# Performance work log

Measured on AMD Instinct MI355X. Metric: run time of the kernel, lower is better.

Reference implementation:

```python
import jax, jax.numpy as jnp
import numpy as np

N, IN, OUT, T = 65536, 256, 256, 8


def setup_inputs() -> dict:
    key = jax.random.key(0)
    k1, k2, k3, k4 = jax.random.split(key, 4)
    x = jax.random.normal(k1, (N, IN), dtype=jnp.float32)
    types = jax.random.randint(k2, (N,), 0, T, dtype=jnp.int32)
    # xavier_uniform for W: limit = sqrt(6 / (fan_in + fan_out)) with fan computed
    # on the last two dims (out_size, in_size)
    limit = float(np.sqrt(6.0 / (IN + OUT)))
    W = jax.random.uniform(k3, (T, OUT, IN), dtype=jnp.float32, minval=-limit, maxval=limit)
    # original inits b to zeros; use small random values so the bias path is exercised
    b = 0.01 * jax.random.normal(k4, (T, OUT), dtype=jnp.float32)
    return {"x": x, "types": types, "W": W, "b": b}


def reference(x, types, W, b):
    # out[i] = W[types[i]] @ x[i] + b[types[i]]
    # Grouped-GEMM expressed as a loop over the small fixed set of types,
    # avoiding the huge [N, OUT, IN] gather of W[types].
    num_types = W.shape[0]
    out = b[types]  # [N, OUT]
    for t in range(num_types):
        mask = (types == t)[:, None]  # [N, 1]
        out = out + jnp.where(mask, x @ W[t].T, jnp.float32(0.0))
    return out
```

## Files before the change

### kernel.cpp

```cpp
#include <hip/hip_runtime.h>
#include <stdint.h>


#define NROWS 65536
#define NTYPES 8
#define KDIM 256
#define ODIM 256
#define BM 32
#define MAX_TILES (NROWS / BM + NTYPES)

typedef __attribute__((ext_vector_type(8))) short short8;
typedef __attribute__((ext_vector_type(4))) float f32x4;

__device__ __forceinline__ unsigned short f2bf(float f) {
    unsigned int u = __float_as_uint(f);
    u += 0x7fffu + ((u >> 16) & 1u);
    return (unsigned short)(u >> 16);
}

__global__ void prep_bucket_kernel(const float* __restrict__ W,
                                   unsigned short* __restrict__ Wp,
                                   const int* __restrict__ types,
                                   int* __restrict__ cnt,
                                   int* __restrict__ idx) {
    const int b = blockIdx.x;
    if (b < 256) {
        const int gid = b * 256 + threadIdx.x;
        const int R   = gid >> 5;
        const int c32 = gid & 31;
        const int t  = R >> 8;
        const int r  = R & 255;
        const int f  = r >> 4;
        const int rr = r & 15;
        const int q  = c32 >> 2;
        const int l  = (c32 & 3) * 16 + rr;
        const float* src = W + (size_t)R * KDIM + c32 * 8;
        const float4 v0 = *(const float4*)src;
        const float4 v1 = *(const float4*)(src + 4);
        ushort4 p0, p1;
        p0.x = f2bf(v0.x); p0.y = f2bf(v0.y); p0.z = f2bf(v0.z); p0.w = f2bf(v0.w);
        p1.x = f2bf(v1.x); p1.y = f2bf(v1.y); p1.z = f2bf(v1.z); p1.w = f2bf(v1.w);
        ushort4* dst = (ushort4*)(Wp + (size_t)(((t * 16 + f) * 8 + q) * 512 + l * 8));
        dst[0] = p0; dst[1] = p1;
    } else {
        __shared__ int h[NTYPES];
        __shared__ int base[NTYPES];
        int i = (b - 256) * 256 + threadIdx.x;
        if (threadIdx.x < NTYPES) h[threadIdx.x] = 0;
        __syncthreads();
        int t = types[i];
        int r = atomicAdd(&h[t], 1);
        __syncthreads();
        if (threadIdx.x < NTYPES)
            base[threadIdx.x] = atomicAdd(&cnt[threadIdx.x], h[threadIdx.x]);
        __syncthreads();
        idx[t * NROWS + base[t] + r] = i;
    }
}

__global__ __launch_bounds__(256, 5)
void gemm_kernel(const float* __restrict__ x,
                 const float* __restrict__ bias,
                 const unsigned short* __restrict__ Wp,
                 const int* __restrict__ cnt,
                 const int* __restrict__ idx,
                 float* __restrict__ out) {
    const int bid = blockIdx.x;
    int t = -1, m0 = 0, count = 0, accum = 0;
    #pragma unroll
    for (int i = 0; i < NTYPES; ++i) {
        int c = cnt[i];
        int ntile = (c + BM - 1) / BM;
        if (t < 0 && bid < accum + ntile) { t = i; m0 = (bid - accum) * BM; count = c; }
        accum += ntile;
    }
    if (t < 0) return;

    __shared__ unsigned short As[BM * KDIM];
    __shared__ int idx_s[BM];
    char* AsB = (char*)As;

    const int tid = threadIdx.x;
    const int srow = tid >> 3;
    const int sc   = tid & 7;

    {
        const int gr = m0 + srow;
        const int xr = idx[t * NROWS + (gr < count ? gr : count - 1)];
        if (sc == 0) idx_s[srow] = xr;
        const float* xs = x + (size_t)xr * KDIM;
        float4 av[8];
        #pragma unroll
        for (int s = 0; s < 8; ++s)
            av[s] = *(const float4*)(xs + (s * 8 + sc) * 4);
        #pragma unroll
        for (int s = 0; s < 8; ++s) {
            const int slot = s * 8 + sc;
            ushort4 pk;
            pk.x = f2bf(av[s].x); pk.y = f2bf(av[s].y);
            pk.z = f2bf(av[s].z); pk.w = f2bf(av[s].w);
            const int c = slot >> 1;
            *(ushort4*)(AsB + srow * 512 + ((c ^ (srow & 7)) * 16) + (slot & 1) * 8) = pk;
        }
    }
    __syncthreads();

    const int wave = tid >> 6;
    const int lane = tid & 63;
    const int lr = lane & 15;
    const int lq = lane >> 4;

    const unsigned short* Wpt = Wp + (size_t)t * 16 * 8 * 512;

    f32x4 acc[2][4] = {};

    #pragma unroll
    for (int q = 0; q < 8; ++q) {
        short8 bf[4], af[2];
        #pragma unroll
        for (int j = 0; j < 4; ++j)
            bf[j] = *(const short8*)(Wpt + ((size_t)((wave * 4 + j) * 8 + q)) * 512
                                         + lane * 8);
        #pragma unroll
        for (int i = 0; i < 2; ++i) {
            const int row = i * 16 + lr;
            af[i] = *(const short8*)(AsB + row * 512
                                         + (((q << 2) + lq) ^ (row & 7)) * 16);
        }
        #pragma unroll
        for (int i = 0; i < 2; ++i)
            #pragma unroll
            for (int j = 0; j < 4; ++j)
                acc[i][j] = __builtin_amdgcn_mfma_f32_16x16x32_bf16(
                    af[i], bf[j], acc[i][j], 0, 0, 0);
    }

    float bv[4];
    #pragma unroll
    for (int j = 0; j < 4; ++j)
        bv[j] = bias[t * ODIM + wave * 64 + j * 16 + lr];

    #pragma unroll
    for (int i = 0; i < 2; ++i) {
        #pragma unroll
        for (int r = 0; r < 4; ++r) {
            const int lm = i * 16 + lq * 4 + r;
            const int gr = m0 + lm;
            if (gr < count) {
                const size_t orow = (size_t)idx_s[lm] * ODIM;
                #pragma unroll
                for (int j = 0; j < 4; ++j)
                    __builtin_nontemporal_store(
                        acc[i][j][r] + bv[j],
                        &out[orow + wave * 64 + j * 16 + lr]);
            }
        }
    }
}

extern "C" void kernel_launch(void* const* d_in, const int* in_sizes, int n_in,
                              void* d_out, int out_size, void* d_ws, size_t ws_size,
                              hipStream_t stream) {
    const float* x     = (const float*)d_in[0];
    const int*   types = (const int*)d_in[1];
    const float* W     = (const float*)d_in[2];
    const float* b     = (const float*)d_in[3];
    float* out = (float*)d_out;

    char* ws = (char*)d_ws;
    int* cnt = (int*)ws;
    int* idx = (int*)(ws + 1024);
    unsigned short* Wp = (unsigned short*)(ws + 1024 + (size_t)NTYPES * NROWS * sizeof(int));

    hipMemsetAsync(cnt, 0, NTYPES * sizeof(int), stream);
    prep_bucket_kernel<<<512, 256, 0, stream>>>(W, Wp, types, cnt, idx);
    gemm_kernel<<<MAX_TILES, 256, 0, stream>>>(x, b, Wp, cnt, idx, out);
}
```

Before: 135.3 us.

## Replace global type bucketing with per-block local sort over contiguous row tiles

New measurement: 143.3 us. 5.9% more time.

```diff
diff --git a/kernel.cpp b/kernel.cpp
--- a/kernel.cpp
+++ b/kernel.cpp
@@ -6,8 +6,9 @@
 #define NTYPES 8
 #define KDIM 256
 #define ODIM 256
-#define BM 32
-#define MAX_TILES (NROWS / BM + NTYPES)
+#define RPB 128
+#define NBLK (NROWS / RPB)
+#define MAXFRAG 16
 
 typedef __attribute__((ext_vector_type(8))) short short8;
 typedef __attribute__((ext_vector_type(4))) float f32x4;
@@ -18,141 +19,147 @@
     return (unsigned short)(u >> 16);
 }
 
-__global__ void prep_bucket_kernel(const float* __restrict__ W,
-                                   unsigned short* __restrict__ Wp,
-                                   const int* __restrict__ types,
-                                   int* __restrict__ cnt,
-                                   int* __restrict__ idx) {
-    const int b = blockIdx.x;
-    if (b < 256) {
-        const int gid = b * 256 + threadIdx.x;
-        const int R   = gid >> 5;
-        const int c32 = gid & 31;
-        const int t  = R >> 8;
-        const int r  = R & 255;
-        const int f  = r >> 4;
-        const int rr = r & 15;
-        const int q  = c32 >> 2;
-        const int l  = (c32 & 3) * 16 + rr;
-        const float* src = W + (size_t)R * KDIM + c32 * 8;
-        const float4 v0 = *(const float4*)src;
-        const float4 v1 = *(const float4*)(src + 4);
-        ushort4 p0, p1;
-        p0.x = f2bf(v0.x); p0.y = f2bf(v0.y); p0.z = f2bf(v0.z); p0.w = f2bf(v0.w);
-        p1.x = f2bf(v1.x); p1.y = f2bf(v1.y); p1.z = f2bf(v1.z); p1.w = f2bf(v1.w);
-        ushort4* dst = (ushort4*)(Wp + (size_t)(((t * 16 + f) * 8 + q) * 512 + l * 8));
-        dst[0] = p0; dst[1] = p1;
-    } else {
-        __shared__ int h[NTYPES];
-        __shared__ int base[NTYPES];
-        int i = (b - 256) * 256 + threadIdx.x;
-        if (threadIdx.x < NTYPES) h[threadIdx.x] = 0;
-        __syncthreads();
-        int t = types[i];
-        int r = atomicAdd(&h[t], 1);
-        __syncthreads();
-        if (threadIdx.x < NTYPES)
-            base[threadIdx.x] = atomicAdd(&cnt[threadIdx.x], h[threadIdx.x]);
-        __syncthreads();
-        idx[t * NROWS + base[t] + r] = i;
-    }
+__global__ void prep_pack_kernel(const float* __restrict__ W,
+                                 unsigned short* __restrict__ Wp) {
+    const int gid = blockIdx.x * 256 + threadIdx.x;
+    const int R   = gid >> 5;
+    const int c32 = gid & 31;
+    const int t  = R >> 8;
+    const int r  = R & 255;
+    const int f  = r >> 4;
+    const int rr = r & 15;
+    const int q  = c32 >> 2;
+    const int l  = (c32 & 3) * 16 + rr;
+    const float* src = W + (size_t)R * KDIM + c32 * 8;
+    const float4 v0 = *(const float4*)src;
+    const float4 v1 = *(const float4*)(src + 4);
+    ushort4 p0, p1;
+    p0.x = f2bf(v0.x); p0.y = f2bf(v0.y); p0.z = f2bf(v0.z); p0.w = f2bf(v0.w);
+    p1.x = f2bf(v1.x); p1.y = f2bf(v1.y); p1.z = f2bf(v1.z); p1.w = f2bf(v1.w);
+    ushort4* dst = (ushort4*)(Wp + (size_t)(((t * 16 + f) * 8 + q) * 512 + l * 8));
+    dst[0] = p0; dst[1] = p1;
 }
 
-__global__ __launch_bounds__(256, 5)
+__global__ __launch_bounds__(256, 2)
 void gemm_kernel(const float* __restrict__ x,
                  const float* __restrict__ bias,
                  const unsigned short* __restrict__ Wp,
-                 const int* __restrict__ cnt,
-                 const int* __restrict__ idx,
+                 const int* __restrict__ types,
                  float* __restrict__ out) {
-    const int bid = blockIdx.x;
-    int t = -1, m0 = 0, count = 0, accum = 0;
-    #pragma unroll
-    for (int i = 0; i < NTYPES; ++i) {
-        int c = cnt[i];
-        int ntile = (c + BM - 1) / BM;
-        if (t < 0 && bid < accum + ntile) { t = i; m0 = (bid - accum) * BM; count = c; }
-        accum += ntile;
-    }
-    if (t < 0) return;
+    const int w0 = blockIdx.x * RPB;
 
-    __shared__ unsigned short As[BM * KDIM];
-    __shared__ int idx_s[BM];
+    __shared__ unsigned short As[RPB * KDIM];
+    __shared__ int perm[RPB];
+    __shared__ int hist[NTYPES];
+    __shared__ int base_[NTYPES];
+    __shared__ int ftype[MAXFRAG];
+    __shared__ int fbase[MAXFRAG];
+    __shared__ int fcnt_[MAXFRAG];
+    __shared__ int nfrag_s;
     char* AsB = (char*)As;
 
     const int tid = threadIdx.x;
-    const int srow = tid >> 3;
-    const int sc   = tid & 7;
+
+    if (tid < NTYPES) hist[tid] = 0;
+    __syncthreads();
+
+    int myt = 0, myrank = 0;
+    if (tid < RPB) {
+        myt = types[w0 + tid];
+        myrank = atomicAdd(&hist[myt], 1);
+    }
 
     {
-        const int gr = m0 + srow;
-        const int xr = idx[t * NROWS + (gr < count ? gr : count - 1)];
-        if (sc == 0) idx_s[srow] = xr;
-        const float* xs = x + (size_t)xr * KDIM;
-        float4 av[8];
+        const int srow = tid >> 1;
+        const int sh   = tid & 1;
+        const float* xs = x + (size_t)(w0 + srow) * KDIM + sh * 128;
         #pragma unroll
-        for (int s = 0; s < 8; ++s)
-            av[s] = *(const float4*)(xs + (s * 8 + sc) * 4);
-        #pragma unroll
-        for (int s = 0; s < 8; ++s) {
-            const int slot = s * 8 + sc;
-            ushort4 pk;
-            pk.x = f2bf(av[s].x); pk.y = f2bf(av[s].y);
-            pk.z = f2bf(av[s].z); pk.w = f2bf(av[s].w);
-            const int c = slot >> 1;
-            *(ushort4*)(AsB + srow * 512 + ((c ^ (srow & 7)) * 16) + (slot & 1) * 8) = pk;
+        for (int rnd = 0; rnd < 4; ++rnd) {
+            float4 av[8];
+            #pragma unroll
+            for (int s = 0; s < 8; ++s)
+                av[s] = *(const float4*)(xs + (rnd * 8 + s) * 4);
+            #pragma unroll
+            for (int s = 0; s < 8; ++s) {
+                const int slot = sh * 32 + rnd * 8 + s;
+                ushort4 pk;
+                pk.x = f2bf(av[s].x); pk.y = f2bf(av[s].y);
+                pk.z = f2bf(av[s].z); pk.w = f2bf(av[s].w);
+                const int c = slot >> 1;
+                *(ushort4*)(AsB + srow * 512 + ((c ^ (srow & 7)) * 16)
+                            + (slot & 1) * 8) = pk;
+            }
         }
     }
+    __syncthreads();
+
+    if (tid == 0) {
+        int acc = 0, nf = 0;
+        #pragma unroll
+        for (int t2 = 0; t2 < NTYPES; ++t2) {
+            base_[t2] = acc;
+            const int c = hist[t2];
+            for (int f = 0; f < c; f += 16) {
+                ftype[nf] = t2;
+                fbase[nf] = acc + f;
+                fcnt_[nf] = (c - f < 16) ? (c - f) : 16;
+                ++nf;
+            }
+            acc += c;
+        }
+        nfrag_s = nf;
+    }
+    __syncthreads();
+    if (tid < RPB) perm[base_[myt] + myrank] = tid;
     __syncthreads();
 
     const int wave = tid >> 6;
     const int lane = tid & 63;
     const int lr = lane & 15;
     const int lq = lane >> 4;
+    const int nfrag = nfrag_s;
 
-    const unsigned short* Wpt = Wp + (size_t)t * 16 * 8 * 512;
+    short8 bf[8][4];
+    float bv[4];
+    int cur_t = -1;
 
-    f32x4 acc[2][4] = {};
-
-    #pragma unroll
-    for (int q = 0; q < 8; ++q) {
-        short8 bf[4], af[2];
-        #pragma unroll
-        for (int j = 0; j < 4; ++j)
-            bf[j] = *(const short8*)(Wpt + ((size_t)((wave * 4 + j) * 8 + q)) * 512
-                                         + lane * 8);
-        #pragma unroll
-        for (int i = 0; i < 2; ++i) {
-            const int row = i * 16 + lr;
-            af[i] = *(const short8*)(AsB + row * 512
-                                         + (((q << 2) + lq) ^ (row & 7)) * 16);
-        }
-        #pragma unroll
-        for (int i = 0; i < 2; ++i)
+    for (int fi = 0; fi < nfrag; ++fi) {
+        const int t = ftype[fi];
+        if (t != cur_t) {
+            const unsigned short* wbase = Wp + (size_t)t * (16 * 8 * 512)
+                                             + (size_t)(wave * 4) * 8 * 512 + lane * 8;
+            #pragma unroll
+            for (int q = 0; q < 8; ++q)
+                #pragma unroll
+                for (int j = 0; j < 4; ++j)
+                    bf[q][j] = *(const short8*)(wbase + j * 4096 + q * 512);
             #pragma unroll
             for (int j = 0; j < 4; ++j)
-                acc[i][j] = __builtin_amdgcn_mfma_f32_16x16x32_bf16(
-                    af[i], bf[j], acc[i][j], 0, 0, 0);
-    }
+                bv[j] = bias[t * ODIM + wave * 64 + j * 16 + lr];
+            cur_t = t;
+        }
+        const int fb = fbase[fi], fc = fcnt_[fi];
+        const int arow = perm[fb + (lr < fc ? lr : 0)];
 
-    float bv[4];
-    #pragma unroll
-    for (int j = 0; j < 4; ++j)
-        bv[j] = bias[t * ODIM + wave * 64 + j * 16 + lr];
+        f32x4 acc[4] = {};
+        #pragma unroll
+        for (int q = 0; q < 8; ++q) {
+            const short8 af = *(const short8*)(AsB + arow * 512
+                                 + ((((q << 2) + lq) ^ (arow & 7)) * 16));
+            #pragma unroll
+            for (int j = 0; j < 4; ++j)
+                acc[j] = __builtin_amdgcn_mfma_f32_16x16x32_bf16(
+                    af, bf[q][j], acc[j], 0, 0, 0);
+        }
 
-    #pragma unroll
-    for (int i = 0; i < 2; ++i) {
         #pragma unroll
         for (int r = 0; r < 4; ++r) {
-            const int lm = i * 16 + lq * 4 + r;
-            const int gr = m0 + lm;
-            if (gr < count) {
-                const size_t orow = (size_t)idx_s[lm] * ODIM;
+            const int fr = lq * 4 + r;
+            if (fr < fc) {
+                const size_t orow = (size_t)(w0 + perm[fb + fr]) * ODIM;
                 #pragma unroll
                 for (int j = 0; j < 4; ++j)
-                    __builtin_nontemporal_store(
-                        acc[i][j][r] + bv[j],
-                        &out[orow + wave * 64 + j * 16 + lr]);
+                    out[orow + wave * 64 + j * 16 + lr] = acc[j][r] + bv[j];
             }
         }
     }
@@ -167,12 +174,8 @@
     const float* b     = (const float*)d_in[3];
     float* out = (float*)d_out;
 
-    char* ws = (char*)d_ws;
-    int* cnt = (int*)ws;
-    int* idx = (int*)(ws + 1024);
-    unsigned short* Wp = (unsigned short*)(ws + 1024 + (size_t)NTYPES * NROWS * sizeof(int));
+    unsigned short* Wp = (unsigned short*)d_ws;
 
-    hipMemsetAsync(cnt, 0, NTYPES * sizeof(int), stream);
-    prep_bucket_kernel<<<512, 256, 0, stream>>>(W, Wp, types, cnt, idx);
-    gemm_kernel<<<MAX_TILES, 256, 0, stream>>>(x, b, Wp, cnt, idx, out);
+    prep_pack_kernel<<<256, 256, 0, stream>>>(W, Wp);
+    gemm_kernel<<<NBLK, 256, 0, stream>>>(x, b, Wp, types, out);
 }
```
